# Performance work log

Hardware: AMD Instinct MI355X
Metric: run time of the kernel (lower is better)

## Reference

```python
import jax, jax.numpy as jnp
import numpy as np

S, R, CM, H, CA, CZ = 128, 256, 256, 8, 32, 128


def _ln(x, w, b):
    mu = x.mean(-1, keepdims=True)
    var = x.var(-1, keepdims=True)
    return (x - mu) * jax.lax.rsqrt(var + 1e-5) * w + b


def setup_inputs() -> dict:
    key = jax.random.key(0)
    ks = jax.random.split(key, 20)
    n = lambda i, shape: jax.random.normal(ks[i], shape, jnp.float32) * 0.05
    return {
        "m": jax.random.normal(ks[0], (S, R, CM), jnp.float32),
        "m_mask": jnp.ones((S, R), jnp.float32),
        "z": jax.random.normal(ks[1], (R, R, CZ), jnp.float32),
        "row_ln_w": jnp.ones((CM,)), "row_ln_b": jnp.zeros((CM,)),
        "row_z_ln_w": jnp.ones((CZ,)), "row_z_ln_b": jnp.zeros((CZ,)),
        "row_wq": n(2, (CM, H * CA)), "row_wk": n(3, (CM, H * CA)), "row_wv": n(4, (CM, H * CA)),
        "row_wb": n(5, (CZ, H)),
        "row_wg": n(6, (CM, H * CA)), "row_bg": jnp.zeros((H * CA,)),
        "row_wo": n(7, (H * CA, CM)), "row_bo": jnp.zeros((CM,)),
        "col_ln_w": jnp.ones((CM,)), "col_ln_b": jnp.zeros((CM,)),
        "col_wq": n(8, (CM, H * CA)), "col_wk": n(9, (CM, H * CA)), "col_wv": n(10, (CM, H * CA)),
        "col_wg": n(11, (CM, H * CA)), "col_bg": jnp.zeros((H * CA,)),
        "col_wo": n(12, (H * CA, CM)), "col_bo": jnp.zeros((CM,)),
        "tr_ln_w": jnp.ones((CM,)), "tr_ln_b": jnp.zeros((CM,)),
        "tr_w1": n(13, (CM, 4 * CM)), "tr_b1": jnp.zeros((4 * CM,)),
        "tr_w2": n(14, (4 * CM, CM)), "tr_b2": jnp.zeros((CM,)),
    }


def _row_atten(m, m_mask, z, ln_w, ln_b, z_ln_w, z_ln_b, wq, wk, wv, wb, wg, bg, wo, bo):
    # MSA row attention with pair bias: attend over residues within each sequence row.
    x = _ln(m, ln_w, ln_b)                                   # [s,r,cm]
    q = (x @ wq).reshape(S, R, H, CA) * (CA ** -0.5)
    k = (x @ wk).reshape(S, R, H, CA)
    v = (x @ wv).reshape(S, R, H, CA)
    pair_bias = jnp.transpose(_ln(z, z_ln_w, z_ln_b) @ wb, (2, 0, 1))  # [h,r,r]
    mask_bias = (m_mask - 1.0)[:, None, None, :] * 1e9       # [s,1,1,r] over keys
    logits = jnp.einsum('sqhc,skhc->shqk', q, k) + pair_bias[None] + mask_bias
    a = jax.nn.softmax(logits, axis=-1)
    o = jnp.einsum('shqk,skhc->sqhc', a, v)
    g = jax.nn.sigmoid(x @ wg + bg).reshape(S, R, H, CA)
    return (g * o).reshape(S, R, H * CA) @ wo + bo


def _col_atten(m, m_mask, ln_w, ln_b, wq, wk, wv, wg, bg, wo, bo):
    # MSA column attention: attend over sequences within each residue column.
    x = _ln(m, ln_w, ln_b)                                   # [s,r,cm]
    q = (x @ wq).reshape(S, R, H, CA) * (CA ** -0.5)
    k = (x @ wk).reshape(S, R, H, CA)
    v = (x @ wv).reshape(S, R, H, CA)
    mask_bias = (jnp.transpose(m_mask) - 1.0)[:, None, None, :] * 1e9  # [r,1,1,s]
    logits = jnp.einsum('qrhc,krhc->rhqk', q, k) + mask_bias
    a = jax.nn.softmax(logits, axis=-1)
    o = jnp.einsum('rhqk,krhc->qrhc', a, v)
    g = jax.nn.sigmoid(x @ wg + bg).reshape(S, R, H, CA)
    return (g * o).reshape(S, R, H * CA) @ wo + bo


def _transition(m, ln_w, ln_b, w1, b1, w2, b2):
    x = _ln(m, ln_w, ln_b)
    return jax.nn.relu(x @ w1 + b1) @ w2 + b2


def reference(m, m_mask, z,
              row_ln_w, row_ln_b, row_z_ln_w, row_z_ln_b,
              row_wq, row_wk, row_wv, row_wb, row_wg, row_bg, row_wo, row_bo,
              col_ln_w, col_ln_b, col_wq, col_wk, col_wv, col_wg, col_bg, col_wo, col_bo,
              tr_ln_w, tr_ln_b, tr_w1, tr_b1, tr_w2, tr_b2):
    m = m + _row_atten(m, m_mask, z, row_ln_w, row_ln_b, row_z_ln_w, row_z_ln_b,
                       row_wq, row_wk, row_wv, row_wb, row_wg, row_bg, row_wo, row_bo)
    m = m + _col_atten(m, m_mask, col_ln_w, col_ln_b, col_wq, col_wk, col_wv,
                       col_wg, col_bg, col_wo, col_bo)
    m = m + _transition(m, tr_ln_w, tr_ln_b, tr_w1, tr_b1, tr_w2, tr_b2)
    return m
```

## Files before the change

kernel.cpp:

```cpp
#include <hip/hip_runtime.h>
#include <stdint.h>

#define S_ 128
#define R_ 256
#define CM_ 256
#define H_ 8
#define CA_ 32
#define CZ_ 128

typedef unsigned short u16;
typedef __bf16 bf16x8 __attribute__((ext_vector_type(8)));
typedef float f32x4 __attribute__((ext_vector_type(4)));

__device__ __forceinline__ float bf2f(u16 u){ unsigned v = ((unsigned)u) << 16; float f; __builtin_memcpy(&f, &v, 4); return f; }
__device__ __forceinline__ u16 f2bf(float f){ __bf16 h = (__bf16)f; u16 u; __builtin_memcpy(&u, &h, 2); return u; }
__device__ __forceinline__ unsigned pkbf(float lo, float hi){
  unsigned r; asm("v_cvt_pk_bf16_f32 %0, %1, %2" : "=v"(r) : "v"(lo), "v"(hi)); return r;
}

__device__ __forceinline__ void gl16(const void* g, void* l){
  __builtin_amdgcn_global_load_lds((const __attribute__((address_space(1))) void*)g,
                                   (__attribute__((address_space(3))) void*)l, 16, 0, 0);
}

struct WSrc { const float* p[12]; };
__global__ __launch_bounds__(256) void transpose_all(WSrc srcs, u16* __restrict__ dst){
  int b = blockIdx.x, t = threadIdx.x;
  int job, idx;
  if(b < 2560){ job = b >> 8; idx = ((b & 255) << 8) + t; }
  else if(b < 3584){ job = 10; idx = ((b - 2560) << 8) + t; }
  else { job = 11; idx = ((b - 3584) << 8) + t; }
  int K = (job == 11) ? 1024 : 256;
  int N = (job == 10) ? 1024 : 256;
  int off;
  if(job < 10) off = job * 65536;
  else if(job == 10) off = 655360;
  else off = 917504;
  int k = idx / N, n = idx - k * N;
  float sc = (job == 0 || job == 5) ? 0.17677669529663687f : 1.f;
  dst[off + n * K + k] = f2bf(srcs.p[job][idx] * sc);
}

__global__ __launch_bounds__(256) void ln_kernel(const float* __restrict__ in, const float* __restrict__ w,
                          const float* __restrict__ b, u16* __restrict__ out){
  int wv = threadIdx.x >> 6, lane = threadIdx.x & 63;
  long long row = (long long)blockIdx.x * 4 + wv;
  float4 v = ((const float4*)(in + row * CM_))[lane];
  float s = v.x + v.y + v.z + v.w;
  for(int mo = 32; mo; mo >>= 1) s += __shfl_xor(s, mo, 64);
  float mu = s * (1.f / CM_);
  float dx = v.x - mu, dy = v.y - mu, dz = v.z - mu, dw = v.w - mu;
  float s2 = dx * dx + dy * dy + dz * dz + dw * dw;
  for(int mo = 32; mo; mo >>= 1) s2 += __shfl_xor(s2, mo, 64);
  float rstd = rsqrtf(s2 * (1.f / CM_) + 1e-5f);
  float4 w4 = ((const float4*)w)[lane];
  float4 b4 = ((const float4*)b)[lane];
  ushort4 st;
  st.x = f2bf(dx * rstd * w4.x + b4.x);
  st.y = f2bf(dy * rstd * w4.y + b4.y);
  st.z = f2bf(dz * rstd * w4.z + b4.z);
  st.w = f2bf(dw * rstd * w4.w + b4.w);
  *(ushort4*)(out + row * CM_ + lane * 4) = st;
}

__global__ __launch_bounds__(256) void pair_bias_kernel(const float* __restrict__ z, const float* __restrict__ lnw,
                                 const float* __restrict__ lnb, const float* __restrict__ wb,
                                 u16* __restrict__ pb){
  __shared__ __attribute__((aligned(16))) unsigned char Xl[32 * 256];
  __shared__ __attribute__((aligned(16))) unsigned char Wl[16 * 256];
  const int t = threadIdx.x;
  const int wv = t >> 6, lane = t & 63, l15 = lane & 15, l4 = lane >> 4;
  const int r0 = blockIdx.x * 32;

  if(t < 128){
    const float4* wr = (const float4*)(wb + t * 8);
    float4 a = wr[0], bq = wr[1];
    u16 vals[8] = {f2bf(a.x), f2bf(a.y), f2bf(a.z), f2bf(a.w),
                   f2bf(bq.x), f2bf(bq.y), f2bf(bq.z), f2bf(bq.w)};
    #pragma unroll
    for(int n = 0; n < 8; n++){
      *(u16*)(Wl + ((n * 256 + t * 2) ^ ((n & 7) << 4))) = vals[n];
      *(u16*)(Wl + (((n + 8) * 256 + t * 2) ^ ((n & 7) << 4))) = 0;
    }
  }
  {
    int row = wv * 8 + (lane >> 3);
    int c0 = (lane & 7) * 16;
    const float4* rp = (const float4*)(z + (long long)(r0 + row) * CZ_ + c0);
    float4 v0 = rp[0], v1 = rp[1], v2 = rp[2], v3 = rp[3];
    float s = v0.x + v0.y + v0.z + v0.w + v1.x + v1.y + v1.z + v1.w
            + v2.x + v2.y + v2.z + v2.w + v3.x + v3.y + v3.z + v3.w;
    s += __shfl_xor(s, 1, 64); s += __shfl_xor(s, 2, 64); s += __shfl_xor(s, 4, 64);
    float mu = s * (1.f / CZ_);
    float d[16] = {v0.x - mu, v0.y - mu, v0.z - mu, v0.w - mu,
                   v1.x - mu, v1.y - mu, v1.z - mu, v1.w - mu,
                   v2.x - mu, v2.y - mu, v2.z - mu, v2.w - mu,
                   v3.x - mu, v3.y - mu, v3.z - mu, v3.w - mu};
    float s2 = 0.f;
    #pragma unroll
    for(int i = 0; i < 16; i++) s2 += d[i] * d[i];
    s2 += __shfl_xor(s2, 1, 64); s2 += __shfl_xor(s2, 2, 64); s2 += __shfl_xor(s2, 4, 64);
    float rstd = rsqrtf(s2 * (1.f / CZ_) + 1e-5f);
    const float4* wp = (const float4*)(lnw + c0);
    const float4* bp = (const float4*)(lnb + c0);
    float x[16];
    #pragma unroll
    for(int i = 0; i < 4; i++){
      float4 w4 = wp[i], b4 = bp[i];
      x[i * 4 + 0] = d[i * 4 + 0] * rstd * w4.x + b4.x;
      x[i * 4 + 1] = d[i * 4 + 1] * rstd * w4.y + b4.y;
      x[i * 4 + 2] = d[i * 4 + 2] * rstd * w4.z + b4.z;
      x[i * 4 + 3] = d[i * 4 + 3] * rstd * w4.w + b4.w;
    }
    uint4 p0, p1;
    p0.x = pkbf(x[0], x[1]);  p0.y = pkbf(x[2], x[3]);
    p0.z = pkbf(x[4], x[5]);  p0.w = pkbf(x[6], x[7]);
    p1.x = pkbf(x[8], x[9]);  p1.y = pkbf(x[10], x[11]);
    p1.z = pkbf(x[12], x[13]); p1.w = pkbf(x[14], x[15]);
    *(uint4*)(Xl + ((row * 256 + c0 * 2) ^ ((row & 7) << 4))) = p0;
    *(uint4*)(Xl + ((row * 256 + c0 * 2 + 16) ^ ((row & 7) << 4))) = p1;
  }
  __syncthreads();
  if(wv < 2){
    f32x4 acc = {0.f, 0.f, 0.f, 0.f};
    #pragma unroll
    for(int ks = 0; ks < 4; ks++){
      int rowA = wv * 16 + l15;
      bf16x8 a = *(const bf16x8*)(Xl + ((rowA * 256 + l4 * 16 + ks * 64) ^ ((rowA & 7) << 4)));
      bf16x8 b = *(const bf16x8*)(Wl + ((l15 * 256 + l4 * 16 + ks * 64) ^ ((l15 & 7) << 4)));
      acc = __builtin_amdgcn_mfma_f32_16x16x32_bf16(a, b, acc, 0, 0, 0);
    }
    if(l15 < 8){
      #pragma unroll
      for(int r = 0; r < 4; r++){
        int rowg = r0 + wv * 16 + l4 * 4 + r;
        int q = rowg >> 8, k = rowg & 255;
        int off = (((l15 * 16 + (q >> 4)) * 16 + (k >> 4)) << 10)
                + ((((q >> 2) & 3) * 16 + (k & 15)) << 2) + (q & 3);
        pb[off] = f2bf(acc[r]);
      }
    }
  }
}

template<bool HAS_BIAS, bool HAS_SIG, bool RELU, bool RES, bool F32OUT>
__global__ __launch_bounds__(256) void gemm128(
    const u16* __restrict__ A, const u16* __restrict__ Wt,
    const float* __restrict__ bias, const float* __restrict__ res,
    void* __restrict__ outv, int M, int N, int K, int sigStart){
  __shared__ __attribute__((aligned(16))) unsigned char Ab[16384];
  __shared__ __attribute__((aligned(16))) unsigned char Bb[16384];
  const int t = threadIdx.x;
  const int wv = t >> 6, lane = t & 63, l15 = lane & 15, l4 = lane >> 4;
  const int wm = wv >> 1, wn = wv & 1;
  const unsigned flat = blockIdx.y * gridDim.x + blockIdx.x;
  const unsigned NB = gridDim.x, mper = gridDim.y >> 3;
  const unsigned xcd = flat & 7, j = flat >> 3;
  const unsigned n_blk = j % NB, m_blk = xcd * mper + j / NB;
  const long long m0 = (long long)m_blk * 128;
  const int n0 = n_blk * 128;
  const int srow = t >> 3;
  const int ksw  = ((t & 7) ^ (srow & 7)) * 8;
  const u16* Ag = A  + (m0 + srow) * (long long)K + ksw;
  const u16* Bg = Wt + (long long)(n0 + srow) * K + ksw;
  f32x4 acc[4][4] = {};
  for(int kk = 0; kk < K; kk += 64){
    #pragma unroll
    for(int i = 0; i < 4; i++){
      gl16(Ag + (long long)i * 32 * K + kk, Ab + wv * 1024 + lane * 16 + i * 4096);
      gl16(Bg + (long long)i * 32 * K + kk, Bb + wv * 1024 + lane * 16 + i * 4096);
    }
    asm volatile("s_waitcnt vmcnt(0)" ::: "memory");
    __syncthreads();
    #pragma unroll
    for(int kh = 0; kh < 2; kh++){
      bf16x8 af[4], bq[4];
      #pragma unroll
      for(int mt = 0; mt < 4; mt++){
        int rr = wm * 64 + mt * 16 + l15;
        af[mt] = *(const bf16x8*)(Ab + rr * 128 + ((kh * 64 + l4 * 16) ^ ((rr & 7) << 4)));
      }
      #pragma unroll
      for(int nt = 0; nt < 4; nt++){
        int rr = wn * 64 + nt * 16 + l15;
        bq[nt] = *(const bf16x8*)(Bb + rr * 128 + ((kh * 64 + l4 * 16) ^ ((rr & 7) << 4)));
      }
      #pragma unroll
      for(int mt = 0; mt < 4; mt++)
        #pragma unroll
        for(int nt = 0; nt < 4; nt++)
          acc[mt][nt] = __builtin_amdgcn_mfma_f32_16x16x32_bf16(af[mt], bq[nt], acc[mt][nt], 0, 0, 0);
    }
    __syncthreads();
  }
  float bnt[4]; bool sg[4];
  #pragma unroll
  for(int nt = 0; nt < 4; nt++){
    int ncol = n0 + wn * 64 + nt * 16 + l15;
    bnt[nt] = 0.f; sg[nt] = false;
    if(HAS_BIAS){
      if(HAS_SIG){ sg[nt] = (ncol >= sigStart); bnt[nt] = sg[nt] ? bias[ncol - sigStart] : 0.f; }
      else bnt[nt] = bias[ncol];
    }
  }
  #pragma unroll
  for(int mt = 0; mt < 4; mt++){
    #pragma unroll
    for(int r = 0; r < 4; r++){
      long long mrow = m0 + wm * 64 + mt * 16 + l4 * 4 + r;
      #pragma unroll
      for(int nt = 0; nt < 4; nt++){
        int ncol = n0 + wn * 64 + nt * 16 + l15;
        float v = acc[mt][nt][r] + bnt[nt];
        if(HAS_SIG){ if(sg[nt]) v = 1.f / (1.f + __expf(-v)); }
        if(RELU) v = v > 0.f ? v : 0.f;
        if(RES)  v += res[mrow * N + ncol];
        if(F32OUT) ((float*)outv)[mrow * N + ncol] = v;
        else       ((u16*)outv)[mrow * N + ncol] = f2bf(v);
      }
    }
  }
}

template<int L, bool HAS_BIAS>
__global__ __launch_bounds__(256) void atten_kernel(
    const u16* __restrict__ qg, const u16* __restrict__ kg, const u16* __restrict__ vg,
    const u16* __restrict__ gg, const u16* __restrict__ pb, const float* __restrict__ mask,
    u16* __restrict__ og,
    long long obase_mul, long long tstride, long long obase_o, long long ostride,
    long long mbase_mul, int mstride){
  __shared__ __attribute__((aligned(16))) unsigned char smem[L * 128 + 8192];
  unsigned char* Kl = smem;
  unsigned char* Vt = smem + L * 64;
  unsigned char* Pl = smem + L * 128;

  const int t = threadIdx.x;
  const int wv = t >> 6, lane = t & 63, l15 = lane & 15, l4 = lane >> 4;
  const int h = blockIdx.x & 7;
  const int outer = blockIdx.x >> 3;
  const long long base  = (long long)outer * obase_mul + h * CA_;
  const long long baseo = (long long)outer * obase_o  + h * CA_;
  const long long mb = (long long)outer * mbase_mul;
  const int KT = L / 16, NC = L / 64;

  #pragma unroll
  for(int j = 0; j < L * 4; j += 256){
    int cid = j + t;
    int row = cid >> 2, ko = cid & 3;
    int4 kv = *(const int4*)(kg + base + (long long)row * tstride + ko * 8);
    *(int4*)(Kl + ((row * 64 + ko * 16) ^ ((row & 7) << 4))) = kv;
  }
  if(t < L){
    __attribute__((aligned(16))) u16 tmp[32];
    const u16* vp = vg + base + (long long)t * tstride;
    #pragma unroll
    for(int j2 = 0; j2 < 4; j2++) ((int4*)tmp)[j2] = *(const int4*)(vp + j2 * 8);
    int kp = (t >> 6) * 64 + (t & 15) * 4 + ((t >> 4) & 3);
    #pragma unroll
    for(int c = 0; c < 32; c++)
      *(u16*)(Vt + (((c * L + kp) * 2) ^ ((c & 7) << 4))) = tmp[c];
  }
  __syncthreads();

  float mskb[L / 16];
  #pragma unroll
  for(int kt = 0; kt < KT; kt++)
    mskb[kt] = (mask[mb + (long long)(kt * 16 + l15) * mstride] - 1.f) * 1e9f;

  unsigned char* Pw = Pl + wv * 2048;
  const int NQ = L / 4;
  #pragma unroll
  for(int qt = 0; qt < NQ / 16; qt++){
    const int qrow0 = wv * NQ + qt * 16;
    bf16x8 aq = *(const bf16x8*)(qg + base + (long long)(qrow0 + l15) * tstride + l4 * 8);
    f32x4 lac[L / 16];
    #pragma unroll
    for(int kt = 0; kt < KT; kt++){
      int kr = kt * 16 + l15;
      bf16x8 bk = *(const bf16x8*)(Kl + ((kr * 64 + l4 * 16) ^ ((kr & 7) << 4)));
      f32x4 zz = {0.f, 0.f, 0.f, 0.f};
      lac[kt] = __builtin_amdgcn_mfma_f32_16x16x32_bf16(aq, bk, zz, 0, 0, 0);
    }
    const u16* tile = HAS_BIAS ? (pb + (((h * 16 + (qrow0 >> 4)) * 16) << 10) + lane * 4) : nullptr;
    float sm[4] = {1e-30f, 1e-30f, 1e-30f, 1e-30f};
    #pragma unroll
    for(int kt = 0; kt < KT; kt++){
      float mm = mskb[kt];
      if(HAS_BIAS){
        ushort4 b4 = *(const ushort4*)(tile + (kt << 10));
        lac[kt][0] = __expf(lac[kt][0] + mm + bf2f(b4.x));
        lac[kt][1] = __expf(lac[kt][1] + mm + bf2f(b4.y));
        lac[kt][2] = __expf(lac[kt][2] + mm + bf2f(b4.z));
        lac[kt][3] = __expf(lac[kt][3] + mm + bf2f(b4.w));
      } else {
        #pragma unroll
        for(int r = 0; r < 4; r++) lac[kt][r] = __expf(lac[kt][r] + mm);
      }
      #pragma unroll
      for(int r = 0; r < 4; r++) sm[r] += lac[kt][r];
    }
    #pragma unroll
    for(int mo = 1; mo < 16; mo <<= 1)
      #pragma unroll
      for(int r = 0; r < 4; r++) sm[r] += __shfl_xor(sm[r], mo, 64);
    float inv[4];
    #pragma unroll
    for(int r = 0; r < 4; r++) inv[r] = 1.f / sm[r];
    f32x4 oac[2] = {{0,0,0,0},{0,0,0,0}};
    #pragma unroll
    for(int ch = 0; ch < NC; ch++){
      asm volatile("" ::: "memory");
      #pragma unroll
      for(int r = 0; r < 4; r++){
        int qp = l4 * 4 + r;
        uint2 pk2;
        pk2.x = pkbf(lac[ch * 4 + 0][r], lac[ch * 4 + 1][r]);
        pk2.y = pkbf(lac[ch * 4 + 2][r], lac[ch * 4 + 3][r]);
        *(uint2*)(Pw + qp * 128 + ((l15 * 8) ^ ((qp & 7) << 4))) = pk2;
      }
      asm volatile("s_waitcnt lgkmcnt(0)" ::: "memory");
      #pragma unroll
      for(int ksl = 0; ksl < 2; ksl++){
        bf16x8 ap = *(const bf16x8*)(Pw + l15 * 128 + ((ksl * 64 + l4 * 16) ^ ((l15 & 7) << 4)));
        #pragma unroll
        for(int ct = 0; ct < 2; ct++){
          int c = ct * 16 + l15;
          bf16x8 bv = *(const bf16x8*)(Vt + (((c * L + ch * 64 + ksl * 32 + l4 * 8) * 2) ^ ((c & 7) << 4)));
          oac[ct] = __builtin_amdgcn_mfma_f32_16x16x32_bf16(ap, bv, oac[ct], 0, 0, 0);
        }
      }
    }
    #pragma unroll
    for(int ct = 0; ct < 2; ct++)
      #pragma unroll
      for(int r = 0; r < 4; r++){
        int qi = qrow0 + l4 * 4 + r, c = ct * 16 + l15;
        float g = bf2f(gg[base + (long long)qi * tstride + c]);
        og[baseo + (long long)qi * ostride + c] = f2bf(oac[ct][r] * inv[r] * g);
      }
  }
}

extern "C" void kernel_launch(void* const* d_in, const int* in_sizes, int n_in,
                              void* d_out, int out_size, void* d_ws, size_t ws_size,
                              hipStream_t stream){
  const float* m        = (const float*)d_in[0];
  const float* m_mask   = (const float*)d_in[1];
  const float* z        = (const float*)d_in[2];
  const float* row_ln_w = (const float*)d_in[3];
  const float* row_ln_b = (const float*)d_in[4];
  const float* row_z_ln_w = (const float*)d_in[5];
  const float* row_z_ln_b = (const float*)d_in[6];
  const float* row_bg   = (const float*)d_in[12];
  const float* row_bo   = (const float*)d_in[14];
  const float* col_ln_w = (const float*)d_in[15];
  const float* col_ln_b = (const float*)d_in[16];
  const float* col_bg   = (const float*)d_in[21];
  const float* col_bo   = (const float*)d_in[23];
  const float* tr_ln_w  = (const float*)d_in[24];
  const float* tr_ln_b  = (const float*)d_in[25];
  const float* tr_b1    = (const float*)d_in[27];
  const float* tr_b2    = (const float*)d_in[29];
  float* out = (float*)d_out;
  char* ws = (char*)d_ws;

  u16* bx  = (u16*)ws;
  u16* fq  = bx + 8388608;
  u16* t_o = fq + 33554432;
  u16* pb  = t_o + 8388608;
  u16* wt  = pb + 2097152;

  WSrc srcs;
  srcs.p[0] = (const float*)d_in[7];
  srcs.p[1] = (const float*)d_in[8];
  srcs.p[2] = (const float*)d_in[9];
  srcs.p[3] = (const float*)d_in[11];
  srcs.p[4] = (const float*)d_in[13];
  srcs.p[5] = (const float*)d_in[17];
  srcs.p[6] = (const float*)d_in[18];
  srcs.p[7] = (const float*)d_in[19];
  srcs.p[8] = (const float*)d_in[20];
  srcs.p[9] = (const float*)d_in[22];
  srcs.p[10] = (const float*)d_in[26];
  srcs.p[11] = (const float*)d_in[28];

  dim3 b256(256);
  transpose_all<<<dim3(4608), b256, 0, stream>>>(srcs, wt);
  pair_bias_kernel<<<dim3(2048), b256, 0, stream>>>(z, row_z_ln_w, row_z_ln_b,
                                                    (const float*)d_in[10], pb);

  ln_kernel<<<dim3(8192), b256, 0, stream>>>(m, row_ln_w, row_ln_b, bx);
  gemm128<true,true,false,false,false><<<dim3(8,256), b256, 0, stream>>>(
      bx, wt, row_bg, nullptr, fq, 32768, 1024, 256, 768);
  atten_kernel<256,true><<<dim3(1024), b256, 0, stream>>>(
      fq, fq + 256, fq + 512, fq + 768, pb, m_mask, t_o,
      262144, 1024, 65536, 256, 256, 1);
  gemm128<true,false,false,true,true><<<dim3(2,256), b256, 0, stream>>>(
      t_o, wt + 262144, row_bo, m, out, 32768, 256, 256, 0);

  ln_kernel<<<dim3(8192), b256, 0, stream>>>(out, col_ln_w, col_ln_b, bx);
  gemm128<true,true,false,false,false><<<dim3(8,256), b256, 0, stream>>>(
      bx, wt + 327680, col_bg, nullptr, fq, 32768, 1024, 256, 768);
  atten_kernel<128,false><<<dim3(2048), b256, 0, stream>>>(
      fq, fq + 256, fq + 512, fq + 768, nullptr, m_mask, t_o,
      1024, 262144, 256, 65536, 1, 256);
  gemm128<true,false,false,true,true><<<dim3(2,256), b256, 0, stream>>>(
      t_o, wt + 589824, col_bo, out, out, 32768, 256, 256, 0);

  ln_kernel<<<dim3(8192), b256, 0, stream>>>(out, tr_ln_w, tr_ln_b, bx);
  gemm128<true,false,true,false,false><<<dim3(8,256), b256, 0, stream>>>(
      bx, wt + 655360, tr_b1, nullptr, fq, 32768, 1024, 256, 0);
  gemm128<true,false,false,true,true><<<dim3(2,256), b256, 0, stream>>>(
      fq, wt + 917504, tr_b2, out, out, 32768, 256, 1024, 0);
}
```

Before: 283.5 us.

## Split row-attention query blocks, read K from global, fold log2e into exp2

```diff
diff --git a/kernel.cpp b/kernel.cpp
--- a/kernel.cpp
+++ b/kernel.cpp
@@ -12,10 +12,15 @@
 typedef __bf16 bf16x8 __attribute__((ext_vector_type(8)));
 typedef float f32x4 __attribute__((ext_vector_type(4)));
 
+#define LOG2E 1.4426950408889634f
+
 __device__ __forceinline__ float bf2f(u16 u){ unsigned v = ((unsigned)u) << 16; float f; __builtin_memcpy(&f, &v, 4); return f; }
 __device__ __forceinline__ u16 f2bf(float f){ __bf16 h = (__bf16)f; u16 u; __builtin_memcpy(&u, &h, 2); return u; }
 __device__ __forceinline__ unsigned pkbf(float lo, float hi){
   unsigned r; asm("v_cvt_pk_bf16_f32 %0, %1, %2" : "=v"(r) : "v"(lo), "v"(hi)); return r;
+}
+__device__ __forceinline__ float fexp2(float x){
+  float r; asm("v_exp_f32 %0, %1" : "=v"(r) : "v"(x)); return r;
 }
 
 __device__ __forceinline__ void gl16(const void* g, void* l){
@@ -37,7 +42,7 @@
   else if(job == 10) off = 655360;
   else off = 917504;
   int k = idx / N, n = idx - k * N;
-  float sc = (job == 0 || job == 5) ? 0.17677669529663687f : 1.f;
+  float sc = (job == 0 || job == 5) ? (0.17677669529663687f * LOG2E) : 1.f;
   dst[off + n * K + k] = f2bf(srcs.p[job][idx] * sc);
 }
 
@@ -137,7 +142,7 @@
         int q = rowg >> 8, k = rowg & 255;
         int off = (((l15 * 16 + (q >> 4)) * 16 + (k >> 4)) << 10)
                 + ((((q >> 2) & 3) * 16 + (k & 15)) << 2) + (q & 3);
-        pb[off] = f2bf(acc[r]);
+        pb[off] = f2bf(acc[r] * LOG2E);
       }
     }
   }
@@ -222,34 +227,30 @@
   }
 }
 
-template<int L, bool HAS_BIAS>
+template<int L, int SPLIT, bool HAS_BIAS>
 __global__ __launch_bounds__(256) void atten_kernel(
     const u16* __restrict__ qg, const u16* __restrict__ kg, const u16* __restrict__ vg,
     const u16* __restrict__ gg, const u16* __restrict__ pb, const float* __restrict__ mask,
     u16* __restrict__ og,
     long long obase_mul, long long tstride, long long obase_o, long long ostride,
     long long mbase_mul, int mstride){
-  __shared__ __attribute__((aligned(16))) unsigned char smem[L * 128 + 8192];
-  unsigned char* Kl = smem;
-  unsigned char* Vt = smem + L * 64;
-  unsigned char* Pl = smem + L * 128;
+  __shared__ __attribute__((aligned(16))) unsigned char smem[L * 64 + 8192];
+  unsigned char* Vt = smem;
+  unsigned char* Pl = smem + L * 64;
 
   const int t = threadIdx.x;
   const int wv = t >> 6, lane = t & 63, l15 = lane & 15, l4 = lane >> 4;
-  const int h = blockIdx.x & 7;
-  const int outer = blockIdx.x >> 3;
+  const int bid = blockIdx.x;
+  const int h = bid & 7;
+  const int g2 = bid >> 3;
+  const int sp = g2 & (SPLIT - 1);
+  const int outer = g2 / SPLIT;
   const long long base  = (long long)outer * obase_mul + h * CA_;
   const long long baseo = (long long)outer * obase_o  + h * CA_;
   const long long mb = (long long)outer * mbase_mul;
   const int KT = L / 16, NC = L / 64;
-
-  #pragma unroll
-  for(int j = 0; j < L * 4; j += 256){
-    int cid = j + t;
-    int row = cid >> 2, ko = cid & 3;
-    int4 kv = *(const int4*)(kg + base + (long long)row * tstride + ko * 8);
-    *(int4*)(Kl + ((row * 64 + ko * 16) ^ ((row & 7) << 4))) = kv;
-  }
+  const int QB = L / SPLIT;
+
   if(t < L){
     __attribute__((aligned(16))) u16 tmp[32];
     const u16* vp = vg + base + (long long)t * tstride;
@@ -265,19 +266,17 @@
   float mskb[L / 16];
   #pragma unroll
   for(int kt = 0; kt < KT; kt++)
-    mskb[kt] = (mask[mb + (long long)(kt * 16 + l15) * mstride] - 1.f) * 1e9f;
+    mskb[kt] = (mask[mb + (long long)(kt * 16 + l15) * mstride] - 1.f) * (1e9f * LOG2E);
 
   unsigned char* Pw = Pl + wv * 2048;
-  const int NQ = L / 4;
-  #pragma unroll
-  for(int qt = 0; qt < NQ / 16; qt++){
-    const int qrow0 = wv * NQ + qt * 16;
+  #pragma unroll 1
+  for(int qt = 0; qt < QB / 64; qt++){
+    const int qrow0 = sp * QB + wv * (QB / 4) + qt * 16;
     bf16x8 aq = *(const bf16x8*)(qg + base + (long long)(qrow0 + l15) * tstride + l4 * 8);
     f32x4 lac[L / 16];
     #pragma unroll
     for(int kt = 0; kt < KT; kt++){
-      int kr = kt * 16 + l15;
-      bf16x8 bk = *(const bf16x8*)(Kl + ((kr * 64 + l4 * 16) ^ ((kr & 7) << 4)));
+      bf16x8 bk = *(const bf16x8*)(kg + base + (long long)(kt * 16 + l15) * tstride + l4 * 8);
       f32x4 zz = {0.f, 0.f, 0.f, 0.f};
       lac[kt] = __builtin_amdgcn_mfma_f32_16x16x32_bf16(aq, bk, zz, 0, 0, 0);
     }
@@ -288,13 +287,13 @@
       float mm = mskb[kt];
       if(HAS_BIAS){
         ushort4 b4 = *(const ushort4*)(tile + (kt << 10));
-        lac[kt][0] = __expf(lac[kt][0] + mm + bf2f(b4.x));
-        lac[kt][1] = __expf(lac[kt][1] + mm + bf2f(b4.y));
-        lac[kt][2] = __expf(lac[kt][2] + mm + bf2f(b4.z));
-        lac[kt][3] = __expf(lac[kt][3] + mm + bf2f(b4.w));
+        lac[kt][0] = fexp2(lac[kt][0] + mm + bf2f(b4.x));
+        lac[kt][1] = fexp2(lac[kt][1] + mm + bf2f(b4.y));
+        lac[kt][2] = fexp2(lac[kt][2] + mm + bf2f(b4.z));
+        lac[kt][3] = fexp2(lac[kt][3] + mm + bf2f(b4.w));
       } else {
         #pragma unroll
-        for(int r = 0; r < 4; r++) lac[kt][r] = __expf(lac[kt][r] + mm);
+        for(int r = 0; r < 4; r++) lac[kt][r] = fexp2(lac[kt][r] + mm);
       }
       #pragma unroll
       for(int r = 0; r < 4; r++) sm[r] += lac[kt][r];
@@ -392,7 +391,7 @@
   ln_kernel<<<dim3(8192), b256, 0, stream>>>(m, row_ln_w, row_ln_b, bx);
   gemm128<true,true,false,false,false><<<dim3(8,256), b256, 0, stream>>>(
       bx, wt, row_bg, nullptr, fq, 32768, 1024, 256, 768);
-  atten_kernel<256,true><<<dim3(1024), b256, 0, stream>>>(
+  atten_kernel<256,2,true><<<dim3(2048), b256, 0, stream>>>(
       fq, fq + 256, fq + 512, fq + 768, pb, m_mask, t_o,
       262144, 1024, 65536, 256, 256, 1);
   gemm128<true,false,false,true,true><<<dim3(2,256), b256, 0, stream>>>(
@@ -401,7 +400,7 @@
   ln_kernel<<<dim3(8192), b256, 0, stream>>>(out, col_ln_w, col_ln_b, bx);
   gemm128<true,true,false,false,false><<<dim3(8,256), b256, 0, stream>>>(
       bx, wt + 327680, col_bg, nullptr, fq, 32768, 1024, 256, 768);
-  atten_kernel<128,false><<<dim3(2048), b256, 0, stream>>>(
+  atten_kernel<128,1,false><<<dim3(2048), b256, 0, stream>>>(
       fq, fq + 256, fq + 512, fq + 768, nullptr, m_mask, t_o,
       1024, 262144, 256, 65536, 1, 256);
   gemm128<true,false,false,true,true><<<dim3(2,256), b256, 0, stream>>>(
```

Measured after the change: 298.8 us. +5.4%, slower.
